# Kernel tuning notes

Measured on AMD Instinct MI355X. Metric: run time of the kernel, lower is better.

## Reference

```python
import jax, jax.numpy as jnp
import numpy as np

B, T, S, H, L = 64, 512, 400, 768, 9


def setup_inputs() -> dict:
    rng = np.random.default_rng(0)
    attn = np.zeros((B, T), np.int32)
    ids_lens = np.zeros((B, S), np.int32)
    for bi in range(B):
        Lb = int(rng.integers(T // 2, T + 1))  # valid wordpiece count
        lens = []
        rem = Lb
        while rem > 0 and len(lens) < S - 1:
            l = int(min(rng.integers(1, 4), rem))  # 1-3 wordpieces per word
            lens.append(l)
            rem -= l
        if rem > 0:
            lens.append(rem)
        attn[bi, :Lb] = 1
        ids_lens[bi, :len(lens)] = np.asarray(lens, np.int32)
    label_ids = rng.integers(0, L, (B, S)).astype(np.int32)
    label_mask = ids_lens > 0
    key = jax.random.key(0)
    k1, k2 = jax.random.split(key)
    last_enc_out = jax.random.normal(k1, (B, T, H), jnp.float32)
    W = jax.random.normal(k2, (H, L), jnp.float32) * 0.02
    b = jnp.zeros((L,), jnp.float32)
    return {
        'last_enc_out': last_enc_out, 'W': W, 'b': b,
        'attention_mask': jnp.asarray(attn), 'ids_lens': jnp.asarray(ids_lens),
        'label_ids': jnp.asarray(label_ids), 'label_mask': jnp.asarray(label_mask),
    }


def reference(last_enc_out, W, b, attention_mask, ids_lens, label_ids, label_mask):
    Bv, Tv, Hv = last_enc_out.shape
    Sv = ids_lens.shape[1]
    # position of each valid token among the row's valid tokens
    tok_pos = jnp.cumsum(attention_mask, axis=1) - 1            # [B,T]
    cum = jnp.cumsum(ids_lens, axis=1)                          # [B,S] nondecreasing
    # word index for each token: first w with cum[w] > tok_pos
    word_idx = jax.vmap(lambda c, p: jnp.searchsorted(c, p, side='right'))(cum, tok_pos)
    valid = attention_mask > 0
    seg = jnp.where(valid, jnp.arange(Bv)[:, None] * Sv + word_idx, Bv * Sv)  # dump slot for pad
    sums = jax.ops.segment_sum(last_enc_out.reshape(Bv * Tv, Hv), seg.reshape(Bv * Tv),
                               num_segments=Bv * Sv + 1)[:Bv * Sv]
    counts = jnp.maximum(ids_lens.reshape(Bv * Sv), 1).astype(last_enc_out.dtype)
    means = (sums / counts[:, None]).reshape(Bv, Sv, Hv)
    word_mask = ids_lens > 0
    bert_embed = jnp.where(word_mask[:, :, None], means, jnp.zeros((), last_enc_out.dtype))
    # dropout is identity in eval mode
    logits = bert_embed @ W + b                                 # [B,S,L]
    logp = jax.nn.log_softmax(logits, axis=-1)
    nll = -jnp.take_along_axis(logp, label_ids[..., None].astype(jnp.int32), axis=-1)[..., 0]
    mf = label_mask.astype(logits.dtype)
    loss = jnp.sum(nll * mf) / jnp.sum(mf)                      # CE with ignore_index masking
    output = jnp.argmax(logits, axis=-1)
    return loss, output
```

## Files before the change

### kernel.cpp

```cpp
#include <hip/hip_runtime.h>
#include <math.h>

#define Bdim 64
#define Tdim 512
#define Sdim 400
#define Hdim 768
#define Ldim 9
#define PSTRIDE 12

#define PROJ_BLOCKS 1024

template <int CTRL>
__device__ __forceinline__ float dpp_add(float x) {
  int y = __builtin_amdgcn_update_dpp(0, __float_as_int(x), CTRL, 0xF, 0xF, false);
  return x + __int_as_float(y);
}
__device__ __forceinline__ float wave_sum63(float x) {
  x = dpp_add<0x111>(x);
  x = dpp_add<0x112>(x);
  x = dpp_add<0x114>(x);
  x = dpp_add<0x118>(x);
  x = dpp_add<0x142>(x);
  x = dpp_add<0x143>(x);
  return x;
}

__global__ __launch_bounds__(Tdim) void setup_kernel(
    const int* __restrict__ attn, const int* __restrict__ ids_lens,
    int* __restrict__ pos2tok, int* __restrict__ wstart,
    int* __restrict__ nvalid, float* __restrict__ accum,
    unsigned* __restrict__ counter) {
  int b = blockIdx.x;
  int tid = threadIdx.x;
  int lane = tid & 63, wid = tid >> 6;
  __shared__ int wsum[8];
  __shared__ int totsm;

  if (b == 0 && tid < 2) accum[tid] = 0.0f;
  if (b == 0 && tid == 2) *counter = 0u;

  int m = attn[b * Tdim + tid];
  int x = m;
#pragma unroll
  for (int off = 1; off < 64; off <<= 1) {
    int v = __shfl_up(x, off, 64);
    if (lane >= off) x += v;
  }
  if (lane == 63) wsum[wid] = x;
  __syncthreads();
  if (tid < 8) {
    int s = wsum[tid];
    int y = s;
#pragma unroll
    for (int off = 1; off < 8; off <<= 1) {
      int v = __shfl_up(y, off, 64);
      if (tid >= off) y += v;
    }
    wsum[tid] = y - s;
    if (tid == 7) totsm = y;
  }
  __syncthreads();
  int total = totsm;
  x += wsum[wid];
  if (m) {
    pos2tok[b * Tdim + x - 1] = tid;
  } else {
    pos2tok[b * Tdim + total + (tid - x)] = -1;
  }
  if (tid == 0) nvalid[b] = total;
  __syncthreads();

  int len = (tid < Sdim) ? ids_lens[b * Sdim + tid] : 0;
  int x2 = len;
#pragma unroll
  for (int off = 1; off < 64; off <<= 1) {
    int v = __shfl_up(x2, off, 64);
    if (lane >= off) x2 += v;
  }
  if (lane == 63) wsum[wid] = x2;
  __syncthreads();
  if (tid < 8) {
    int s = wsum[tid];
    int y = s;
#pragma unroll
    for (int off = 1; off < 8; off <<= 1) {
      int v = __shfl_up(y, off, 64);
      if (tid >= off) y += v;
    }
    wsum[tid] = y - s;
  }
  __syncthreads();
  x2 += wsum[wid];
  if (tid < Sdim) wstart[b * Sdim + tid] = x2 - len;
}

__global__ __launch_bounds__(256, 3) void proj_kernel(
    const float* __restrict__ enc, const float* __restrict__ W,
    const int* __restrict__ pos2tok, float* __restrict__ proj) {
  int tid = threadIdx.x;
  int lane = tid & 63;
  int wv = blockIdx.x * 4 + (tid >> 6);
  int base = wv * 8;

  float wf[3][4][Ldim];
#pragma unroll
  for (int k = 0; k < 3; ++k)
#pragma unroll
    for (int j = 0; j < 4; ++j) {
      int h = 4 * lane + 256 * k + j;
#pragma unroll
      for (int l = 0; l < Ldim; ++l) wf[k][j][l] = W[(size_t)h * Ldim + l];
    }

  int4 g0 = *(const int4*)(pos2tok + base);
  int4 g1 = *(const int4*)(pos2tok + base + 4);

  const float4* encf4 = (const float4*)enc;

  auto step = [&](int t, int p) {
    if (t < 0) return;
    int b = p >> 9;
    const float4* row = encf4 + ((size_t)(b << 9) + t) * (Hdim / 4);
    float4 x0 = row[lane];
    float4 x1 = row[lane + 64];
    float4 x2 = row[lane + 128];

    float d[Ldim];
#pragma unroll
    for (int l = 0; l < Ldim; ++l) {
      d[l] = x0.x * wf[0][0][l] + x0.y * wf[0][1][l] +
             x0.z * wf[0][2][l] + x0.w * wf[0][3][l] +
             x1.x * wf[1][0][l] + x1.y * wf[1][1][l] +
             x1.z * wf[1][2][l] + x1.w * wf[1][3][l] +
             x2.x * wf[2][0][l] + x2.y * wf[2][1][l] +
             x2.z * wf[2][2][l] + x2.w * wf[2][3][l];
    }
#pragma unroll
    for (int l = 0; l < Ldim; ++l) d[l] = wave_sum63(d[l]);

    if (lane == 63) {
      float4 o0 = make_float4(d[0], d[1], d[2], d[3]);
      float4 o1 = make_float4(d[4], d[5], d[6], d[7]);
      float* dst = proj + (size_t)p * PSTRIDE;
      *(float4*)(dst) = o0;
      *(float4*)(dst + 4) = o1;
      dst[8] = d[8];
    }
  };

  step(g0.x, base + 0);
  step(g0.y, base + 1);
  step(g0.z, base + 2);
  step(g0.w, base + 3);
  step(g1.x, base + 4);
  step(g1.y, base + 5);
  step(g1.z, base + 6);
  step(g1.w, base + 7);
}

__global__ __launch_bounds__(256) void word_kernel(
    const float* __restrict__ proj, const float* __restrict__ bias,
    const int* __restrict__ ids_lens, const int* __restrict__ label_ids,
    const int* __restrict__ wstart, const int* __restrict__ nvalid,
    float* __restrict__ out, float* __restrict__ accum,
    unsigned* __restrict__ counter) {
  int bs = blockIdx.x * 256 + threadIdx.x;
  int b = bs / Sdim;
  int len = ids_lens[bs];

  float s[Ldim];
#pragma unroll
  for (int l = 0; l < Ldim; ++l) s[l] = 0.0f;

  if (len > 0) {
    int start = wstart[bs];
    int nv = nvalid[b];
    for (int j = 0; j < len; ++j) {
      int q = start + j;
      if (q >= nv) break;
      const float* pr = proj + ((size_t)(b << 9) + q) * PSTRIDE;
#pragma unroll
      for (int l = 0; l < Ldim; ++l) s[l] += pr[l];
    }
  }
  float inv = (len > 0) ? 1.0f / (float)len : 0.0f;
  float lg[Ldim];
#pragma unroll
  for (int l = 0; l < Ldim; ++l) lg[l] = s[l] * inv + bias[l];

  int amax = 0;
  float mx = lg[0];
#pragma unroll
  for (int l = 1; l < Ldim; ++l)
    if (lg[l] > mx) { mx = lg[l]; amax = l; }
  out[1 + bs] = (float)amax;

  float nll = 0.0f, cnt = 0.0f;
  if (len > 0) {
    float se = 0.0f;
#pragma unroll
    for (int l = 0; l < Ldim; ++l) se += expf(lg[l] - mx);
    float lse = mx + logf(se);
    int lab = label_ids[bs];
    float ll = lg[0];
#pragma unroll
    for (int l = 1; l < Ldim; ++l) ll = (lab == l) ? lg[l] : ll;
    nll = lse - ll;
    cnt = 1.0f;
  }

#pragma unroll
  for (int off = 32; off > 0; off >>= 1) {
    nll += __shfl_down(nll, off, 64);
    cnt += __shfl_down(cnt, off, 64);
  }
  __shared__ float ss[4], cc[4];
  int wid = threadIdx.x >> 6, lane = threadIdx.x & 63;
  if (lane == 0) { ss[wid] = nll; cc[wid] = cnt; }
  __syncthreads();
  if (threadIdx.x == 0) {
    atomicAdd(&accum[0], ss[0] + ss[1] + ss[2] + ss[3]);
    atomicAdd(&accum[1], cc[0] + cc[1] + cc[2] + cc[3]);
    __threadfence();
    unsigned prev = atomicAdd(counter, 1u);
    if (prev == gridDim.x - 1) {
      __threadfence();
      float S = atomicAdd(&accum[0], 0.0f);
      float C = atomicAdd(&accum[1], 0.0f);
      out[0] = S / C;
    }
  }
}

extern "C" void kernel_launch(void* const* d_in, const int* in_sizes, int n_in,
                              void* d_out, int out_size, void* d_ws, size_t ws_size,
                              hipStream_t stream) {
  const float* enc      = (const float*)d_in[0];
  const float* W        = (const float*)d_in[1];
  const float* bias     = (const float*)d_in[2];
  const int* attn       = (const int*)d_in[3];
  const int* ids_lens   = (const int*)d_in[4];
  const int* label_ids  = (const int*)d_in[5];

  float* out = (float*)d_out;

  char* ws = (char*)d_ws;
  size_t off0 = 0;
  int* pos2tok      = (int*)(ws + off0);      off0 += (size_t)Bdim * Tdim * sizeof(int);
  int* wstart       = (int*)(ws + off0);      off0 += (size_t)Bdim * Sdim * sizeof(int);
  int* nvalid       = (int*)(ws + off0);      off0 += 256;
  float* accum      = (float*)(ws + off0);    off0 += 128;
  unsigned* counter = (unsigned*)(ws + off0); off0 += 128;
  float* proj       = (float*)(ws + off0);    off0 += (size_t)Bdim * Tdim * PSTRIDE * sizeof(float);

  int word_blocks = (Bdim * Sdim) / 256;

  setup_kernel<<<Bdim, Tdim, 0, stream>>>(attn, ids_lens, pos2tok, wstart,
                                          nvalid, accum, counter);
  proj_kernel<<<PROJ_BLOCKS, 256, 0, stream>>>(enc, W, pos2tok, proj);
  word_kernel<<<word_blocks, 256, 0, stream>>>(proj, bias, ids_lens, label_ids,
                                               wstart, nvalid, out, accum, counter);
}
```

Measured before the change: 40.77 us.

## Software-pipeline token loads in projection kernel with double-buffered pairs and fewer blocks

The projection kernel now processes token pairs in a strided loop with two register buffers, so the encoder rows for the next pair are fetched while the current pair is projected and reduced. Validity is checked against nvalid per batch instead of reading -1 sentinels, so setup no longer writes padding entries and pad rows are skipped without a pos2tok lookup. Grid size is halved and the occupancy hint removed, trading parallelism and register pressure (two sets of 6 float4 plus the 108-float weight cache) for latency hiding.

```diff
diff --git a/kernel.cpp b/kernel.cpp
--- a/kernel.cpp
+++ b/kernel.cpp
@@ -8,7 +8,9 @@
 #define Ldim 9
 #define PSTRIDE 12
 
-#define PROJ_BLOCKS 1024
+#define PROJ_BLOCKS 512
+#define NWAVES (PROJ_BLOCKS * 4)
+#define NPAIR 8
 
 template <int CTRL>
 __device__ __forceinline__ float dpp_add(float x) {
@@ -62,11 +64,7 @@
   __syncthreads();
   int total = totsm;
   x += wsum[wid];
-  if (m) {
-    pos2tok[b * Tdim + x - 1] = tid;
-  } else {
-    pos2tok[b * Tdim + total + (tid - x)] = -1;
-  }
+  if (m) pos2tok[b * Tdim + x - 1] = tid;
   if (tid == 0) nvalid[b] = total;
   __syncthreads();
 
@@ -94,13 +92,13 @@
   if (tid < Sdim) wstart[b * Sdim + tid] = x2 - len;
 }
 
-__global__ __launch_bounds__(256, 3) void proj_kernel(
+__global__ __launch_bounds__(256) void proj_kernel(
     const float* __restrict__ enc, const float* __restrict__ W,
-    const int* __restrict__ pos2tok, float* __restrict__ proj) {
+    const int* __restrict__ pos2tok, const int* __restrict__ nvalid,
+    float* __restrict__ proj) {
   int tid = threadIdx.x;
   int lane = tid & 63;
   int wv = blockIdx.x * 4 + (tid >> 6);
-  int base = wv * 8;
 
   float wf[3][4][Ldim];
 #pragma unroll
@@ -112,50 +110,72 @@
       for (int l = 0; l < Ldim; ++l) wf[k][j][l] = W[(size_t)h * Ldim + l];
     }
 
-  int4 g0 = *(const int4*)(pos2tok + base);
-  int4 g1 = *(const int4*)(pos2tok + base + 4);
-
   const float4* encf4 = (const float4*)enc;
 
-  auto step = [&](int t, int p) {
-    if (t < 0) return;
-    int b = p >> 9;
-    const float4* row = encf4 + ((size_t)(b << 9) + t) * (Hdim / 4);
-    float4 x0 = row[lane];
-    float4 x1 = row[lane + 64];
-    float4 x2 = row[lane + 128];
-
-    float d[Ldim];
-#pragma unroll
-    for (int l = 0; l < Ldim; ++l) {
-      d[l] = x0.x * wf[0][0][l] + x0.y * wf[0][1][l] +
-             x0.z * wf[0][2][l] + x0.w * wf[0][3][l] +
-             x1.x * wf[1][0][l] + x1.y * wf[1][1][l] +
-             x1.z * wf[1][2][l] + x1.w * wf[1][3][l] +
-             x2.x * wf[2][0][l] + x2.y * wf[2][1][l] +
-             x2.z * wf[2][2][l] + x2.w * wf[2][3][l];
-    }
-#pragma unroll
-    for (int l = 0; l < Ldim; ++l) d[l] = wave_sum63(d[l]);
-
-    if (lane == 63) {
-      float4 o0 = make_float4(d[0], d[1], d[2], d[3]);
-      float4 o1 = make_float4(d[4], d[5], d[6], d[7]);
-      float* dst = proj + (size_t)p * PSTRIDE;
-      *(float4*)(dst) = o0;
-      *(float4*)(dst + 4) = o1;
-      dst[8] = d[8];
-    }
-  };
-
-  step(g0.x, base + 0);
-  step(g0.y, base + 1);
-  step(g0.z, base + 2);
-  step(g0.w, base + 3);
-  step(g1.x, base + 4);
-  step(g1.y, base + 5);
-  step(g1.z, base + 6);
-  step(g1.w, base + 7);
+  float4 A00, A01, A02, A10, A11, A12;
+  float4 B00, B01, B02, B10, B11, B12;
+  int vA = 0, pA = 0, vB = 0, pB = 0;
+
+#define LOADP(S, K)                                                        \
+  {                                                                        \
+    int p_ = (wv + (K) * NWAVES) * 2;                                      \
+    int b_ = p_ >> 9;                                                      \
+    int q_ = p_ & 511;                                                     \
+    v##S = nvalid[b_] - q_;                                                \
+    p##S = p_;                                                             \
+    if (v##S >= 1) {                                                       \
+      int t_ = pos2tok[p_];                                                \
+      const float4* r_ = encf4 + ((size_t)(b_ << 9) + t_) * (Hdim / 4);    \
+      S##00 = r_[lane]; S##01 = r_[lane + 64]; S##02 = r_[lane + 128];     \
+    }                                                                      \
+    if (v##S >= 2) {                                                       \
+      int t_ = pos2tok[p_ + 1];                                            \
+      const float4* r_ = encf4 + ((size_t)(b_ << 9) + t_) * (Hdim / 4);    \
+      S##10 = r_[lane]; S##11 = r_[lane + 64]; S##12 = r_[lane + 128];     \
+    }                                                                      \
+  }
+
+#define PROJ1(X0, X1, X2, PP)                                              \
+  {                                                                        \
+    float dd[Ldim];                                                        \
+    _Pragma("unroll") for (int l = 0; l < Ldim; ++l) {                     \
+      dd[l] = X0.x * wf[0][0][l] + X0.y * wf[0][1][l] +                    \
+              X0.z * wf[0][2][l] + X0.w * wf[0][3][l] +                    \
+              X1.x * wf[1][0][l] + X1.y * wf[1][1][l] +                    \
+              X1.z * wf[1][2][l] + X1.w * wf[1][3][l] +                    \
+              X2.x * wf[2][0][l] + X2.y * wf[2][1][l] +                    \
+              X2.z * wf[2][2][l] + X2.w * wf[2][3][l];                     \
+    }                                                                      \
+    _Pragma("unroll") for (int l = 0; l < Ldim; ++l) dd[l] = wave_sum63(dd[l]); \
+    if (lane == 63) {                                                      \
+      float* dst_ = proj + (size_t)(PP) * PSTRIDE;                         \
+      *(float4*)(dst_) = make_float4(dd[0], dd[1], dd[2], dd[3]);          \
+      *(float4*)(dst_ + 4) = make_float4(dd[4], dd[5], dd[6], dd[7]);      \
+      dst_[8] = dd[8];                                                     \
+    }                                                                      \
+  }
+
+#define COMPP(S)                                                           \
+  {                                                                        \
+    if (v##S >= 1) PROJ1(S##00, S##01, S##02, p##S);                       \
+    if (v##S >= 2) PROJ1(S##10, S##11, S##12, p##S + 1);                   \
+  }
+
+  LOADP(A, 0)
+  LOADP(B, 1)
+#pragma unroll
+  for (int k = 0; k < NPAIR; ++k) {
+    if (k & 1) {
+      COMPP(B)
+      if (k + 2 < NPAIR) LOADP(B, k + 2)
+    } else {
+      COMPP(A)
+      if (k + 2 < NPAIR) LOADP(A, k + 2)
+    }
+  }
+#undef LOADP
+#undef PROJ1
+#undef COMPP
 }
 
 __global__ __launch_bounds__(256) void word_kernel(
@@ -257,7 +277,7 @@
 
   setup_kernel<<<Bdim, Tdim, 0, stream>>>(attn, ids_lens, pos2tok, wstart,
                                           nvalid, accum, counter);
-  proj_kernel<<<PROJ_BLOCKS, 256, 0, stream>>>(enc, W, pos2tok, proj);
+  proj_kernel<<<PROJ_BLOCKS, 256, 0, stream>>>(enc, W, pos2tok, nvalid, proj);
   word_kernel<<<word_blocks, 256, 0, stream>>>(proj, bias, ids_lens, label_ids,
                                                wstart, nvalid, out, accum, counter);
 }
```

Result: faster. 39.85 us (-2.3%).

## Split projection labels across waves and double-buffer token row loads

Applied to the files above, without the earlier changes.

Each proj block now handles 16 consecutive tokens of a single batch row, with three waves that each compute 3 of the 9 label dot products. This cuts per-wave W registers and reduction work. Token rows are prefetched two ahead in a double buffer so loads overlap the FMAs and DPP reductions. Blocks past the row's valid count exit early, so pad slots no longer need -1 entries in pos2tok. The trade-off is that each encoder row is loaded by three waves instead of one, which relies on cache hits to avoid tripling memory traffic.

```diff
diff --git a/kernel.cpp b/kernel.cpp
--- a/kernel.cpp
+++ b/kernel.cpp
@@ -8,7 +8,8 @@
 #define Ldim 9
 #define PSTRIDE 12
 
-#define PROJ_BLOCKS 1024
+#define PROJ_BLOCKS 2048
+#define TOK_PER_BLK 16
 
 template <int CTRL>
 __device__ __forceinline__ float dpp_add(float x) {
@@ -62,11 +63,7 @@
   __syncthreads();
   int total = totsm;
   x += wsum[wid];
-  if (m) {
-    pos2tok[b * Tdim + x - 1] = tid;
-  } else {
-    pos2tok[b * Tdim + total + (tid - x)] = -1;
-  }
+  if (m) pos2tok[b * Tdim + x - 1] = tid;
   if (tid == 0) nvalid[b] = total;
   __syncthreads();
 
@@ -94,68 +91,75 @@
   if (tid < Sdim) wstart[b * Sdim + tid] = x2 - len;
 }
 
-__global__ __launch_bounds__(256, 3) void proj_kernel(
+__global__ __launch_bounds__(192, 4) void proj_kernel(
     const float* __restrict__ enc, const float* __restrict__ W,
-    const int* __restrict__ pos2tok, float* __restrict__ proj) {
+    const int* __restrict__ pos2tok, const int* __restrict__ nvalid,
+    float* __restrict__ proj) {
   int tid = threadIdx.x;
   int lane = tid & 63;
-  int wv = blockIdx.x * 4 + (tid >> 6);
-  int base = wv * 8;
-
-  float wf[3][4][Ldim];
+  int w = tid >> 6;
+  int l0 = w * 3;
+  int base = blockIdx.x * TOK_PER_BLK;
+  int b = base >> 9;
+  int vc = nvalid[b] - (base & 511);
+  vc = vc < 0 ? 0 : (vc > TOK_PER_BLK ? TOK_PER_BLK : vc);
+  if (vc == 0) return;
+
+  float wf[3][4][3];
 #pragma unroll
   for (int k = 0; k < 3; ++k)
 #pragma unroll
     for (int j = 0; j < 4; ++j) {
       int h = 4 * lane + 256 * k + j;
 #pragma unroll
-      for (int l = 0; l < Ldim; ++l) wf[k][j][l] = W[(size_t)h * Ldim + l];
-    }
-
-  int4 g0 = *(const int4*)(pos2tok + base);
-  int4 g1 = *(const int4*)(pos2tok + base + 4);
-
-  const float4* encf4 = (const float4*)enc;
-
-  auto step = [&](int t, int p) {
-    if (t < 0) return;
-    int b = p >> 9;
-    const float4* row = encf4 + ((size_t)(b << 9) + t) * (Hdim / 4);
-    float4 x0 = row[lane];
-    float4 x1 = row[lane + 64];
-    float4 x2 = row[lane + 128];
-
-    float d[Ldim];
-#pragma unroll
-    for (int l = 0; l < Ldim; ++l) {
-      d[l] = x0.x * wf[0][0][l] + x0.y * wf[0][1][l] +
-             x0.z * wf[0][2][l] + x0.w * wf[0][3][l] +
-             x1.x * wf[1][0][l] + x1.y * wf[1][1][l] +
-             x1.z * wf[1][2][l] + x1.w * wf[1][3][l] +
-             x2.x * wf[2][0][l] + x2.y * wf[2][1][l] +
-             x2.z * wf[2][2][l] + x2.w * wf[2][3][l];
-    }
-#pragma unroll
-    for (int l = 0; l < Ldim; ++l) d[l] = wave_sum63(d[l]);
-
-    if (lane == 63) {
-      float4 o0 = make_float4(d[0], d[1], d[2], d[3]);
-      float4 o1 = make_float4(d[4], d[5], d[6], d[7]);
-      float* dst = proj + (size_t)p * PSTRIDE;
-      *(float4*)(dst) = o0;
-      *(float4*)(dst + 4) = o1;
-      dst[8] = d[8];
-    }
-  };
-
-  step(g0.x, base + 0);
-  step(g0.y, base + 1);
-  step(g0.z, base + 2);
-  step(g0.w, base + 3);
-  step(g1.x, base + 4);
-  step(g1.y, base + 5);
-  step(g1.z, base + 6);
-  step(g1.w, base + 7);
+      for (int c = 0; c < 3; ++c) wf[k][j][c] = W[(size_t)h * Ldim + l0 + c];
+    }
+
+  const float4* encb = (const float4*)enc + (size_t)(b << 9) * (Hdim / 4);
+
+  float4 xr[2][3];
+#pragma unroll
+  for (int i = 0; i < 2; ++i) {
+    int tv = pos2tok[base + i];
+    int t = (i < vc) ? tv : 0;
+    const float4* r = encb + (size_t)t * (Hdim / 4);
+    xr[i][0] = r[lane];
+    xr[i][1] = r[lane + 64];
+    xr[i][2] = r[lane + 128];
+  }
+
+#pragma unroll
+  for (int i = 0; i < TOK_PER_BLK; ++i) {
+    float4 x0 = xr[i & 1][0], x1 = xr[i & 1][1], x2 = xr[i & 1][2];
+    if (i < vc) {
+      float dd[3];
+#pragma unroll
+      for (int c = 0; c < 3; ++c) {
+        dd[c] = x0.x * wf[0][0][c] + x0.y * wf[0][1][c] +
+                x0.z * wf[0][2][c] + x0.w * wf[0][3][c] +
+                x1.x * wf[1][0][c] + x1.y * wf[1][1][c] +
+                x1.z * wf[1][2][c] + x1.w * wf[1][3][c] +
+                x2.x * wf[2][0][c] + x2.y * wf[2][1][c] +
+                x2.z * wf[2][2][c] + x2.w * wf[2][3][c];
+      }
+#pragma unroll
+      for (int c = 0; c < 3; ++c) dd[c] = wave_sum63(dd[c]);
+      if (lane == 63) {
+        float* dst = proj + (size_t)(base + i) * PSTRIDE + l0;
+        dst[0] = dd[0];
+        dst[1] = dd[1];
+        dst[2] = dd[2];
+      }
+    }
+    if (i + 2 < TOK_PER_BLK) {
+      int tv = pos2tok[base + i + 2];
+      int t = (i + 2 < vc) ? tv : 0;
+      const float4* r = encb + (size_t)t * (Hdim / 4);
+      xr[i & 1][0] = r[lane];
+      xr[i & 1][1] = r[lane + 64];
+      xr[i & 1][2] = r[lane + 128];
+    }
+  }
 }
 
 __global__ __launch_bounds__(256) void word_kernel(
@@ -257,7 +261,7 @@
 
   setup_kernel<<<Bdim, Tdim, 0, stream>>>(attn, ids_lens, pos2tok, wstart,
                                           nvalid, accum, counter);
-  proj_kernel<<<PROJ_BLOCKS, 256, 0, stream>>>(enc, W, pos2tok, proj);
+  proj_kernel<<<PROJ_BLOCKS, 192, 0, stream>>>(enc, W, pos2tok, nvalid, proj);
   word_kernel<<<word_blocks, 256, 0, stream>>>(proj, bias, ids_lens, label_ids,
                                                wstart, nvalid, out, accum, counter);
 }
```

New measurement: 39.32 us. -3.6%, faster.
